# Kernel optimization log

Measured on AMD Instinct MI355X. Metric: run time of the kernel, lower is better.

The kernel has to match this reference:

```python
import jax, jax.numpy as jnp
import numpy as np

DIM = 1024
NUM_HEADS = 16
HEAD_DIM = DIM // NUM_HEADS  # 64
SCALE = float(np.sqrt(HEAD_DIM))


def setup_inputs() -> dict:
    key = jax.random.key(0)
    k1, k2, k3, k4 = jax.random.split(key, 4)
    B, N = 2, 2048
    x = jax.random.normal(k1, (B, N, DIM), dtype=jnp.float32)
    # torch nn.Linear weights are [out_features, in_features]
    w_qkv = jax.random.normal(k2, (3 * DIM, DIM), dtype=jnp.float32) * (1.0 / np.sqrt(DIM))
    w_proj = jax.random.normal(k3, (DIM, DIM), dtype=jnp.float32) * (1.0 / np.sqrt(DIM))
    b_proj = jax.random.normal(k4, (DIM,), dtype=jnp.float32) * 0.02
    return {"x": x, "w_qkv": w_qkv, "w_proj": w_proj, "b_proj": b_proj}


def reference(x, w_qkv, w_proj, b_proj):
    B, N, C = x.shape
    H, D = NUM_HEADS, HEAD_DIM
    # qkv linear (no bias): [B,N,3C]
    qkv = jnp.einsum('bnc,oc->bno', x, w_qkv)
    qkv = qkv.reshape(B, N, 3, H, D).transpose(2, 0, 3, 1, 4)  # [3,B,H,N,D]
    q, k, v = qkv[0], qkv[1], qkv[2]
    attn = jnp.einsum('bhnd,bhmd->bhnm', q, k) / SCALE  # [B,H,N,N]
    attn = jax.nn.softmax(attn, axis=-1)
    out = jnp.einsum('bhnm,bhmd->bhnd', attn, v)  # [B,H,N,D]
    out = out.transpose(0, 2, 1, 3).reshape(B, N, C)
    return jnp.einsum('bnc,oc->bno', out, w_proj) + b_proj
```

## Files before the change

kernel.cpp:

```cpp
#include <hip/hip_runtime.h>


typedef __bf16 bf16x8 __attribute__((ext_vector_type(8)));
typedef __bf16 bf16x4 __attribute__((ext_vector_type(4)));
typedef float f32x4 __attribute__((ext_vector_type(4)));

#define NTOK 2048
#define MFMA16(a, b, c) __builtin_amdgcn_mfma_f32_16x16x32_bf16((a), (b), (c), 0, 0, 0)

__device__ __forceinline__ unsigned short f2bf(float f) {
    unsigned int u = __float_as_uint(f);
    u = (u + 0x7FFFu + ((u >> 16) & 1u)) >> 16;
    return (unsigned short)u;
}

__device__ __forceinline__ float hw_exp2(float x) {
#if __has_builtin(__builtin_amdgcn_exp2f)
    return __builtin_amdgcn_exp2f(x);
#else
    float r;
    asm("v_exp_f32 %0, %1" : "=v"(r) : "v"(x));
    return r;
#endif
}

__device__ __forceinline__ void gload16(const void* g, void* l) {
    __builtin_amdgcn_global_load_lds(
        (__attribute__((address_space(1))) void*)(g),
        (__attribute__((address_space(3))) void*)(l), 16, 0, 0);
}

__global__ __launch_bounds__(256) void cast3_kernel(
    const float* __restrict__ x, const float* __restrict__ wq,
    const float* __restrict__ wp, unsigned short* __restrict__ xb,
    unsigned short* __restrict__ wqb, unsigned short* __restrict__ wpb) {
    const int NX = 1048576, NWQ = 786432;
    int i = blockIdx.x * 256 + threadIdx.x;
    const float* src;
    unsigned short* dst;
    int j;
    if (i < NX) { src = x; dst = xb; j = i; }
    else if (i < NX + NWQ) { src = wq; dst = wqb; j = i - NX; }
    else { src = wp; dst = wpb; j = i - NX - NWQ; }
    const float4 v = reinterpret_cast<const float4*>(src)[j];
    ushort4 o;
    o.x = f2bf(v.x); o.y = f2bf(v.y); o.z = f2bf(v.z); o.w = f2bf(v.w);
    reinterpret_cast<ushort4*>(dst)[j] = o;
}

template <int EPI>
__global__ __launch_bounds__(256) void gemm_bt_kernel(
    const unsigned short* __restrict__ A, const unsigned short* __restrict__ B,
    int K, int Ncols,
    unsigned short* __restrict__ q_out, unsigned short* __restrict__ k_out,
    unsigned short* __restrict__ vt_out,
    float* __restrict__ c_out, const float* __restrict__ bias) {
    __shared__ __align__(16) unsigned short ldsA[2][128 * 32];
    __shared__ __align__(16) unsigned short ldsB[2][128 * 32];
    const int tid = threadIdx.x;
    const int l = tid & 63;
    const int wid = tid >> 6;
    const int wr = wid >> 1, wc = wid & 1;
    const int m0 = blockIdx.x * 128, n0 = blockIdx.y * 128;

    f32x4 acc[4][4] = {};

    const int srow = tid >> 2;
    const int sc16 = tid & 3;

    auto STAGE = [&](int buf, int kt) {
#pragma unroll
        for (int r = 0; r < 2; ++r) {
            const int row = r * 64 + srow;
            const int c16 = sc16 ^ (row & 3);
            gload16(A + (size_t)(m0 + row) * K + kt + c16 * 8,
                    (char*)ldsA[buf] + wid * 1024 + r * 4096);
            gload16(B + (size_t)(n0 + row) * K + kt + c16 * 8,
                    (char*)ldsB[buf] + wid * 1024 + r * 4096);
        }
    };

    STAGE(0, 0);
    __syncthreads();

    const int NK = K >> 5;
    int cur = 0;
    for (int ki = 0; ki < NK; ++ki) {
        if (ki + 1 < NK) STAGE(cur ^ 1, (ki + 1) * 32);
        bf16x8 af[4], bfr[4];
#pragma unroll
        for (int m = 0; m < 4; ++m) {
            const int row = wr * 64 + m * 16 + (l & 15);
            const int c16 = (l >> 4) ^ (row & 3);
            af[m] = *(const bf16x8*)((const char*)ldsA[cur] + row * 64 + c16 * 16);
        }
#pragma unroll
        for (int n = 0; n < 4; ++n) {
            const int row = wc * 64 + n * 16 + (l & 15);
            const int c16 = (l >> 4) ^ (row & 3);
            bfr[n] = *(const bf16x8*)((const char*)ldsB[cur] + row * 64 + c16 * 16);
        }
#pragma unroll
        for (int m = 0; m < 4; ++m)
#pragma unroll
            for (int n = 0; n < 4; ++n)
                acc[m][n] = MFMA16(af[m], bfr[n], acc[m][n]);
        __syncthreads();
        cur ^= 1;
    }

#pragma unroll
    for (int m = 0; m < 4; ++m) {
        const int gmb = m0 + wr * 64 + m * 16 + ((l >> 4) << 2);
#pragma unroll
        for (int n = 0; n < 4; ++n) {
            const int gn = n0 + wc * 64 + n * 16 + (l & 15);
            if (EPI == 0) {
                const int which = gn >> 10;
                const int h = (gn >> 6) & 15, d = gn & 63;
#pragma unroll
                for (int r = 0; r < 4; ++r) {
                    const int gm = gmb + r;
                    const int head = ((gm >> 11) << 4) | h;
                    const int t = gm & 2047;
                    const float v = acc[m][n][r];
                    if (which == 0)
                        q_out[((size_t)head * NTOK + t) * 64 + d] =
                            f2bf(v * 0.18033688011f);
                    else if (which == 1)
                        k_out[((size_t)head * NTOK + t) * 64 + d] = f2bf(v);
                    else {
                        const int k6 = t & 63;
                        const int tp = (t & ~63) | (k6 & 0x23) |
                                       ((k6 & 0x0C) << 1) | ((k6 & 0x10) >> 2);
                        vt_out[((size_t)head * 64 + d) * NTOK + tp] = f2bf(v);
                    }
                }
            } else {
                const float bv = bias[gn];
#pragma unroll
                for (int r = 0; r < 4; ++r)
                    c_out[(size_t)(gmb + r) * Ncols + gn] = acc[m][n][r] + bv;
            }
        }
    }
}

__global__ __launch_bounds__(256) void attn_kernel(
    const unsigned short* __restrict__ Qb, const unsigned short* __restrict__ Kb,
    const unsigned short* __restrict__ Vt, unsigned short* __restrict__ Ob) {
    __shared__ __align__(16) unsigned short ldsK[2][64 * 64];
    __shared__ __align__(16) unsigned short ldsV[2][64 * 64];

    const int tid = threadIdx.x, l = tid & 63, wid = tid >> 6;
    const int c = l & 15, g = l >> 4;
    const int head = blockIdx.x;
    const int q0 = blockIdx.y * 64 + wid * 16;

    const unsigned short* Qh = Qb + (size_t)head * NTOK * 64;
    const unsigned short* Kh = Kb + (size_t)head * NTOK * 64;
    const unsigned short* Vh = Vt + (size_t)head * 64 * NTOK;

    bf16x8 qf[2];
#pragma unroll
    for (int kk = 0; kk < 2; ++kk)
        qf[kk] = *(const bf16x8*)(Qh + (size_t)(q0 + c) * 64 + kk * 32 + g * 8);

    f32x4 o_acc[4] = {};
    f32x4 lsum = {};

    const int srow = tid >> 3;

    auto STAGE = [&](int buf, int kbase) {
#pragma unroll
        for (int r = 0; r < 2; ++r) {
            const int row = r * 32 + srow;
            const int slot = (tid & 7) ^ (row & 7);
            gload16(Kh + (size_t)(kbase + row) * 64 + slot * 8,
                    (char*)ldsK[buf] + wid * 1024 + r * 4096);
            gload16(Vh + (size_t)row * NTOK + kbase + slot * 8,
                    (char*)ldsV[buf] + wid * 1024 + r * 4096);
        }
    };

    STAGE(0, 0);
    __syncthreads();

    int cur = 0;
    for (int it = 0; it < 32; ++it) {
        if (it + 1 < 32) STAGE(cur ^ 1, (it + 1) * 64);

        f32x4 s[4] = {};
#pragma unroll
        for (int mk = 0; mk < 4; ++mk) {
            const int row = mk * 16 + c;
#pragma unroll
            for (int kk = 0; kk < 2; ++kk) {
                const int slot = (kk * 4 + g) ^ (row & 7);
                const bf16x8 kf =
                    *(const bf16x8*)((const char*)ldsK[cur] + row * 128 + slot * 16);
                s[mk] = MFMA16(kf, qf[kk], s[mk]);
            }
        }

        bf16x8 pkw[2];
#pragma unroll
        for (int mk = 0; mk < 4; ++mk) {
            const float p0 = hw_exp2(s[mk][0]);
            const float p1 = hw_exp2(s[mk][1]);
            const float p2 = hw_exp2(s[mk][2]);
            const float p3 = hw_exp2(s[mk][3]);
            lsum[0] += p0; lsum[1] += p1; lsum[2] += p2; lsum[3] += p3;
            const int kv = mk >> 1, hh = (mk & 1) * 4;
            pkw[kv][hh + 0] = (__bf16)p0; pkw[kv][hh + 1] = (__bf16)p1;
            pkw[kv][hh + 2] = (__bf16)p2; pkw[kv][hh + 3] = (__bf16)p3;
        }

#pragma unroll
        for (int dm = 0; dm < 4; ++dm) {
            const int row = dm * 16 + c;
#pragma unroll
            for (int kv = 0; kv < 2; ++kv) {
                const int slot = (kv * 4 + g) ^ (row & 7);
                const bf16x8 vt =
                    *(const bf16x8*)((const char*)ldsV[cur] + row * 128 + slot * 16);
                o_acc[dm] = MFMA16(vt, pkw[kv], o_acc[dm]);
            }
        }
        __syncthreads();
        cur ^= 1;
    }

    float lr = (lsum[0] + lsum[1]) + (lsum[2] + lsum[3]);
    lr += __shfl_xor(lr, 16);
    lr += __shfl_xor(lr, 32);

    const int b = head >> 4, h = head & 15;
    const float inv = 1.f / lr;
    unsigned short* orow = Ob + ((size_t)b * NTOK + q0 + c) * 1024 + h * 64;
#pragma unroll
    for (int dm = 0; dm < 4; ++dm) {
        bf16x4 ov;
#pragma unroll
        for (int r = 0; r < 4; ++r) ov[r] = (__bf16)(o_acc[dm][r] * inv);
        *(bf16x4*)(orow + dm * 16 + g * 4) = ov;
    }
}

extern "C" void kernel_launch(void* const* d_in, const int* in_sizes, int n_in,
                              void* d_out, int out_size, void* d_ws, size_t ws_size,
                              hipStream_t stream) {
    const float* x = (const float*)d_in[0];
    const float* w_qkv = (const float*)d_in[1];
    const float* w_proj = (const float*)d_in[2];
    const float* b_proj = (const float*)d_in[3];
    float* out = (float*)d_out;

    char* ws = (char*)d_ws;
    const size_t MB = 1 << 20;
    unsigned short* xb = (unsigned short*)(ws);
    unsigned short* wqkvb = (unsigned short*)(ws + 8 * MB);
    unsigned short* wpb = (unsigned short*)(ws + 14 * MB);
    unsigned short* Qb = (unsigned short*)(ws + 16 * MB);
    unsigned short* Kb = (unsigned short*)(ws + 24 * MB);
    unsigned short* Vt = (unsigned short*)(ws + 32 * MB);
    unsigned short* attnb = xb;

    cast3_kernel<<<8192, 256, 0, stream>>>(x, w_qkv, w_proj, xb, wqkvb, wpb);

    gemm_bt_kernel<0><<<dim3(32, 24), 256, 0, stream>>>(
        xb, wqkvb, 1024, 3072, Qb, Kb, Vt, nullptr, nullptr);

    attn_kernel<<<dim3(32, 32), 256, 0, stream>>>(Qb, Kb, Vt, attnb);

    gemm_bt_kernel<1><<<dim3(32, 8), 256, 0, stream>>>(
        attnb, wpb, 1024, 1024, nullptr, nullptr, nullptr, out, b_proj);
}
```

Baseline: 126.3 us.

## Use 8-wave GEMM blocks and stage V-transpose epilogue through LDS

The GEMM kernel moves from 4 waves to 8 waves per 128x128 tile, so each wave computes a 64x32 sub-tile and issues a single global-to-LDS load per operand per K-step. For the V portion of the QKV projection, results are first written into swizzled shared memory and then stored to the transposed, permuted Vt layout as contiguous 8-byte vectors. This replaces the scattered 2-byte strided stores of the old epilogue. It adds an extra LDS round trip and barrier in that epilogue, and raises the register and launch-bounds configuration for both GEMMs.

```diff
diff --git a/kernel.cpp b/kernel.cpp
--- a/kernel.cpp
+++ b/kernel.cpp
@@ -49,35 +49,29 @@
 }
 
 template <int EPI>
-__global__ __launch_bounds__(256) void gemm_bt_kernel(
+__global__ __launch_bounds__(512) void gemm_bt_kernel(
     const unsigned short* __restrict__ A, const unsigned short* __restrict__ B,
     int K, int Ncols,
     unsigned short* __restrict__ q_out, unsigned short* __restrict__ k_out,
     unsigned short* __restrict__ vt_out,
     float* __restrict__ c_out, const float* __restrict__ bias) {
-    __shared__ __align__(16) unsigned short ldsA[2][128 * 32];
-    __shared__ __align__(16) unsigned short ldsB[2][128 * 32];
+    __shared__ __align__(16) char smem[32768];
     const int tid = threadIdx.x;
     const int l = tid & 63;
     const int wid = tid >> 6;
-    const int wr = wid >> 1, wc = wid & 1;
+    const int c = l & 15, g = l >> 4;
+    const int wr = wid >> 2, wc = wid & 3;
     const int m0 = blockIdx.x * 128, n0 = blockIdx.y * 128;
 
-    f32x4 acc[4][4] = {};
+    f32x4 acc[4][2] = {};
 
     const int srow = tid >> 2;
-    const int sc16 = tid & 3;
-
+    const int sc16 = (tid & 3) ^ (srow & 3);
     auto STAGE = [&](int buf, int kt) {
-#pragma unroll
-        for (int r = 0; r < 2; ++r) {
-            const int row = r * 64 + srow;
-            const int c16 = sc16 ^ (row & 3);
-            gload16(A + (size_t)(m0 + row) * K + kt + c16 * 8,
-                    (char*)ldsA[buf] + wid * 1024 + r * 4096);
-            gload16(B + (size_t)(n0 + row) * K + kt + c16 * 8,
-                    (char*)ldsB[buf] + wid * 1024 + r * 4096);
-        }
+        gload16(A + (size_t)(m0 + srow) * K + kt + sc16 * 8,
+                smem + buf * 8192 + wid * 1024);
+        gload16(B + (size_t)(n0 + srow) * K + kt + sc16 * 8,
+                smem + 16384 + buf * 8192 + wid * 1024);
     };
 
     STAGE(0, 0);
@@ -87,34 +81,68 @@
     int cur = 0;
     for (int ki = 0; ki < NK; ++ki) {
         if (ki + 1 < NK) STAGE(cur ^ 1, (ki + 1) * 32);
-        bf16x8 af[4], bfr[4];
+        bf16x8 af[4], bfr[2];
 #pragma unroll
         for (int m = 0; m < 4; ++m) {
-            const int row = wr * 64 + m * 16 + (l & 15);
-            const int c16 = (l >> 4) ^ (row & 3);
-            af[m] = *(const bf16x8*)((const char*)ldsA[cur] + row * 64 + c16 * 16);
-        }
-#pragma unroll
-        for (int n = 0; n < 4; ++n) {
-            const int row = wc * 64 + n * 16 + (l & 15);
-            const int c16 = (l >> 4) ^ (row & 3);
-            bfr[n] = *(const bf16x8*)((const char*)ldsB[cur] + row * 64 + c16 * 16);
+            const int row = wr * 64 + m * 16 + c;
+            const int c16 = g ^ (row & 3);
+            af[m] = *(const bf16x8*)(smem + cur * 8192 + row * 64 + c16 * 16);
+        }
+#pragma unroll
+        for (int n = 0; n < 2; ++n) {
+            const int row = wc * 32 + n * 16 + c;
+            const int c16 = g ^ (row & 3);
+            bfr[n] = *(const bf16x8*)(smem + 16384 + cur * 8192 + row * 64 + c16 * 16);
         }
 #pragma unroll
         for (int m = 0; m < 4; ++m)
 #pragma unroll
-            for (int n = 0; n < 4; ++n)
+            for (int n = 0; n < 2; ++n)
                 acc[m][n] = MFMA16(af[m], bfr[n], acc[m][n]);
         __syncthreads();
         cur ^= 1;
     }
 
+    if (EPI == 0 && n0 >= 2048) {
+#pragma unroll
+        for (int m = 0; m < 4; ++m) {
+            const int tl0 = wr * 64 + m * 16 + g * 4;
+#pragma unroll
+            for (int n = 0; n < 2; ++n) {
+                const int oc = wc * 32 + n * 16 + c;
+                bf16x4 pv;
+#pragma unroll
+                for (int r = 0; r < 4; ++r) pv[r] = (__bf16)acc[m][n][r];
+                *(bf16x4*)(smem + oc * 256 + ((tl0 * 2) ^ ((oc & 7) << 4))) = pv;
+            }
+        }
+        __syncthreads();
+        const int b = m0 >> 11;
+        const int mloc = m0 & 2047;
+#pragma unroll
+        for (int qq = 0; qq < 4; ++qq) {
+            const int ci = qq * 512 + tid;
+            const int oc = ci >> 4, j16 = ci & 15;
+            const int o = n0 + oc;
+            const int head = b * 16 + ((o >> 6) & 15), d = o & 63;
+            const bf16x4* src = (const bf16x4*)(smem + oc * 256 +
+                                                ((j16 * 16) ^ ((oc & 7) << 4)));
+            const int tl8 = j16 * 8;
+            const int tpb = (tl8 & ~63) | (tl8 & 0x20) | ((tl8 & 0x10) >> 2) |
+                            ((tl8 & 0x08) << 1);
+            unsigned short* orow = vt_out + ((size_t)head * 64 + d) * NTOK + mloc;
+            *(bf16x4*)(orow + tpb) = src[0];
+            *(bf16x4*)(orow + tpb + 8) = src[1];
+        }
+        return;
+    }
+
 #pragma unroll
     for (int m = 0; m < 4; ++m) {
-        const int gmb = m0 + wr * 64 + m * 16 + ((l >> 4) << 2);
-#pragma unroll
-        for (int n = 0; n < 4; ++n) {
-            const int gn = n0 + wc * 64 + n * 16 + (l & 15);
+        const int gmb = m0 + wr * 64 + m * 16 + (g << 2);
+#pragma unroll
+        for (int n = 0; n < 2; ++n) {
+            const int gn = n0 + wc * 32 + n * 16 + c;
             if (EPI == 0) {
                 const int which = gn >> 10;
                 const int h = (gn >> 6) & 15, d = gn & 63;
@@ -127,14 +155,8 @@
                     if (which == 0)
                         q_out[((size_t)head * NTOK + t) * 64 + d] =
                             f2bf(v * 0.18033688011f);
-                    else if (which == 1)
+                    else
                         k_out[((size_t)head * NTOK + t) * 64 + d] = f2bf(v);
-                    else {
-                        const int k6 = t & 63;
-                        const int tp = (t & ~63) | (k6 & 0x23) |
-                                       ((k6 & 0x0C) << 1) | ((k6 & 0x10) >> 2);
-                        vt_out[((size_t)head * 64 + d) * NTOK + tp] = f2bf(v);
-                    }
                 }
             } else {
                 const float bv = bias[gn];
@@ -268,11 +290,11 @@
 
     cast3_kernel<<<8192, 256, 0, stream>>>(x, w_qkv, w_proj, xb, wqkvb, wpb);
 
-    gemm_bt_kernel<0><<<dim3(32, 24), 256, 0, stream>>>(
+    gemm_bt_kernel<0><<<dim3(32, 24), 512, 0, stream>>>(
         xb, wqkvb, 1024, 3072, Qb, Kb, Vt, nullptr, nullptr);
 
     attn_kernel<<<dim3(32, 32), 256, 0, stream>>>(Qb, Kb, Vt, attnb);
 
-    gemm_bt_kernel<1><<<dim3(32, 8), 256, 0, stream>>>(
+    gemm_bt_kernel<1><<<dim3(32, 8), 512, 0, stream>>>(
         attnb, wpb, 1024, 1024, nullptr, nullptr, nullptr, out, b_proj);
 }
```

New measurement: 117.1 us. 1.08x faster.
